# Performance work log

Measured on AMD Instinct MI355X. Metric: run time of the kernel, lower is better.

The kernel has to match this reference:

```python
import jax, jax.numpy as jnp
import numpy as np

B, NT, NZ, NX, NREC = 4, 256, 192, 192, 128
DT, DH = 0.001, 10.0


def setup_inputs() -> dict:
    key = jax.random.key(0)
    k1, k2, k3, k4 = jax.random.split(key, 4)
    # source wavelets, one trace per shot
    x = jax.random.normal(k1, (B, NT, 1), dtype=jnp.float32) * 1e2
    # realistic elastic media
    vp = 2500.0 + 1000.0 * jax.random.uniform(k2, (NZ, NX), dtype=jnp.float32)
    vs = vp / 1.78
    rho = 2000.0 + 300.0 * jax.random.uniform(k3, (NZ, NX), dtype=jnp.float32)
    # per-shot source location (z=5 near surface, random x)
    src_x = jax.random.randint(k4, (B,), 10, NX - 10)
    src_loc = jnp.stack([jnp.full((B,), 5), src_x], axis=1).astype(jnp.int32)
    # receiver line at depth z=5
    rec_x = jnp.linspace(10, NX - 10, NREC).astype(jnp.int32)
    rec_loc = jnp.stack([jnp.full((NREC,), 5, dtype=jnp.int32), rec_x], axis=1)
    return {"x": x, "vp": vp, "vs": vs, "rho": rho,
            "src_loc": src_loc, "rec_loc": rec_loc}


# staggered-grid first differences (forward / backward), zero-padded at edges
def _dxf(f):
    return jnp.pad(jnp.diff(f, axis=-1), ((0, 0), (0, 0), (0, 1))) / DH

def _dxb(f):
    return jnp.pad(jnp.diff(f, axis=-1), ((0, 0), (0, 0), (1, 0))) / DH

def _dzf(f):
    return jnp.pad(jnp.diff(f, axis=-2), ((0, 0), (0, 1), (0, 0))) / DH

def _dzb(f):
    return jnp.pad(jnp.diff(f, axis=-2), ((0, 0), (1, 0), (0, 0))) / DH


def _propagate(x, vp, vs, rho, src_loc, rec_loc):
    lam = rho * (vp ** 2 - 2.0 * vs ** 2)
    mu = rho * vs ** 2
    lam2mu = lam + 2.0 * mu
    buoy = DT / rho  # buoyancy * dt
    bidx = jnp.arange(B)
    sz, sx = src_loc[:, 0], src_loc[:, 1]
    rz, rx = rec_loc[:, 0], rec_loc[:, 1]

    def step(carry, wav_t):
        vx, vz, txx, tzz, txz = carry
        # velocity update from stress divergence
        vx = vx + buoy * (_dxf(txx) + _dzb(txz))
        vz = vz + buoy * (_dxb(txz) + _dzf(tzz))
        # stress update from velocity gradients
        dvxdx = _dxb(vx)
        dvzdz = _dzb(vz)
        txx = txx + DT * (lam2mu * dvxdx + lam * dvzdz)
        tzz = tzz + DT * (lam * dvxdx + lam2mu * dvzdz)
        txz = txz + DT * mu * (_dzf(vx) + _dxf(vz))
        # explosive source injection into txx, tzz (source_type = ['txx','tzz'])
        txx = txx.at[bidx, sz, sx].add(wav_t)
        tzz = tzz.at[bidx, sz, sx].add(wav_t)
        # probe extraction: (B, NREC)
        return (vx, vz, txx, tzz, txz), (vx[:, rz, rx], vz[:, rz, rx])

    z = jnp.zeros((B, NZ, NX), dtype=vp.dtype)
    _, (rvx, rvz) = jax.lax.scan(step, (z, z, z, z, z), x[:, :, 0].T)
    # torch: stack(dim=1) -> (B,NT,NREC); permute(1,2,0) -> (NT,NREC,B); cat dim=2
    y_vx = jnp.transpose(rvx, (0, 2, 1))  # (NT, NREC, B)
    y_vz = jnp.transpose(rvz, (0, 2, 1))
    return jnp.concatenate([y_vx, y_vz], axis=2)  # (NT, NREC, 2B)


def reference(x, vp, vs, rho, src_loc, rec_loc):
    return _propagate(x, vp, vs, rho, src_loc, rec_loc)
```

## Files before the change

kernel.cpp:

```cpp
#include <hip/hip_runtime.h>

#pragma clang fp contract(off)

#define B_    4
#define NT_   256
#define NZ_   192
#define NX_   192
#define NREC_ 128
#define DT_   0.001f
#define DH_   10.0f

#define N_CELL  (NZ_ * NX_)
#define N_FIELD (B_ * N_CELL)

#define K_     4
#define ROWS   4
#define NTHR   1024
#define VH     (2 * K_ - 1)
#define SH     (2 * K_)
#define VROWS  (ROWS + 2 * VH)
#define SROWS  (ROWS + 2 * SH)
#define TILES  (NZ_ / ROWS)
#define NBLK   (B_ * TILES)
#define LDS_BYTES ((2 * VROWS + 3 * SROWS) * NX_ * 4)

__device__ __forceinline__ int imax_(int a, int b) { return a > b ? a : b; }
__device__ __forceinline__ int imin_(int a, int b) { return a < b ? a : b; }

__global__ void mat_kernel(const float* __restrict__ vp, const float* __restrict__ vs,
                           const float* __restrict__ rho,
                           float* __restrict__ lam, float* __restrict__ dtmu,
                           float* __restrict__ lam2mu, float* __restrict__ buoy) {
    int i = blockIdx.x * blockDim.x + threadIdx.x;
    if (i >= N_CELL) return;
    float vpi = vp[i], vsi = vs[i], rhoi = rho[i];
    float vs2 = vsi * vsi;
    float mui = rhoi * vs2;
    float lami = rhoi * (vpi * vpi - 2.0f * vs2);
    lam[i] = lami;
    dtmu[i] = DT_ * mui;
    lam2mu[i] = lami + 2.0f * mui;
    buoy[i] = DT_ / rhoi;
}

template<int S>
__device__ __forceinline__ void substep(
    int tid, int z0, int base, int zv0, int zs0, int sz, int sx, int b, int t0,
    float* __restrict__ vxl, float* __restrict__ vzl,
    float* __restrict__ txxl, float* __restrict__ tzzl, float* __restrict__ txzl,
    const float* __restrict__ lam, const float* __restrict__ dtmu,
    const float* __restrict__ l2m, const float* __restrict__ buoy,
    const float* __restrict__ wav,
    bool rec_ok, int rec_idx, float* __restrict__ out,
    float* __restrict__ vxw, float* __restrict__ vzw,
    float* __restrict__ txxw, float* __restrict__ tzzw, float* __restrict__ txzw) {
    const int t = t0 + S;

    {
        constexpr int hv = 2 * (K_ - 1 - S) + 1;
        constexpr int IV = ((ROWS + 2 * hv) * NX_ + NTHR - 1) / NTHR;
        const int zlo = imax_(0, z0 - hv);
        const int zhi = imin_(NZ_ - 1, z0 + ROWS - 1 + hv);
        const int n   = (zhi - zlo + 1) * NX_;
#pragma unroll
        for (int it = 0; it < IV; ++it) {
            int idx = tid + it * NTHR;
            if (idx < n) {
                int dz = idx / NX_;
                int x  = idx - dz * NX_;
                int z  = zlo + dz;
                int zs = (z - zs0) * NX_ + x;
                int zr = (z - zv0) * NX_ + x;
                float txx_c = txxl[zs];
                float txz_c = txzl[zs];
                float dxf_txx = (x < NX_ - 1) ? (txxl[zs + 1] - txx_c) / DH_ : 0.0f;
                float dzb_txz = (z >= 1)      ? (txz_c - txzl[zs - NX_]) / DH_ : 0.0f;
                float dxb_txz = (x >= 1)      ? (txz_c - txzl[zs - 1]) / DH_ : 0.0f;
                float dzf_tzz = (z < NZ_ - 1) ? (tzzl[zs + NX_] - tzzl[zs]) / DH_ : 0.0f;
                float bu = buoy[z * NX_ + x];
                float nvx = vxl[zr] + bu * (dxf_txx + dzb_txz);
                float nvz = vzl[zr] + bu * (dxb_txz + dzf_tzz);
                vxl[zr] = nvx;
                vzl[zr] = nvz;
                if (S == K_ - 1) {
                    if (z >= z0 && z < z0 + ROWS) {
                        int g = base + z * NX_ + x;
                        vxw[g] = nvx;
                        vzw[g] = nvz;
                    }
                }
            }
        }
    }
    __syncthreads();

    if (rec_ok) {
        size_t o = ((size_t)t * NREC_ + tid) * (2 * B_);
        out[o + b]      = vxl[rec_idx];
        out[o + B_ + b] = vzl[rec_idx];
    }

    {
        constexpr int hs = 2 * (K_ - 1 - S);
        constexpr int IS = ((ROWS + 2 * hs) * NX_ + NTHR - 1) / NTHR;
        const int zlo = imax_(0, z0 - hs);
        const int zhi = imin_(NZ_ - 1, z0 + ROWS - 1 + hs);
        const int n   = (zhi - zlo + 1) * NX_;
#pragma unroll
        for (int it = 0; it < IS; ++it) {
            int idx = tid + it * NTHR;
            if (idx < n) {
                int dz = idx / NX_;
                int x  = idx - dz * NX_;
                int z  = zlo + dz;
                int zs = (z - zs0) * NX_ + x;
                int zr = (z - zv0) * NX_ + x;
                float vx_c = vxl[zr];
                float vz_c = vzl[zr];
                float dvxdx  = (x >= 1)      ? (vx_c - vxl[zr - 1]) / DH_ : 0.0f;
                float dvzdz  = (z >= 1)      ? (vz_c - vzl[zr - NX_]) / DH_ : 0.0f;
                float dzf_vx = (z < NZ_ - 1) ? (vxl[zr + NX_] - vx_c) / DH_ : 0.0f;
                float dxf_vz = (x < NX_ - 1) ? (vzl[zr + 1] - vz_c) / DH_ : 0.0f;
                int c = z * NX_ + x;
                float l  = lam[c];
                float lm = l2m[c];
                float ntxx = txxl[zs] + DT_ * (lm * dvxdx + l * dvzdz);
                float ntzz = tzzl[zs] + DT_ * (l * dvxdx + lm * dvzdz);
                float ntxz = txzl[zs] + dtmu[c] * (dzf_vx + dxf_vz);
                if (z == sz && x == sx) {
                    float w = wav[b * NT_ + t];
                    ntxx = ntxx + w;
                    ntzz = ntzz + w;
                }
                txxl[zs] = ntxx;
                tzzl[zs] = ntzz;
                txzl[zs] = ntxz;
                if (S == K_ - 1) {
                    int g = base + c;
                    txxw[g] = ntxx;
                    tzzw[g] = ntzz;
                    txzw[g] = ntxz;
                }
            }
        }
    }
    __syncthreads();
}

__global__ void __launch_bounds__(NTHR, 4)
step_kernel(const float* __restrict__ vxr, const float* __restrict__ vzr,
            const float* __restrict__ txxr, const float* __restrict__ tzzr,
            const float* __restrict__ txzr,
            float* __restrict__ vxw, float* __restrict__ vzw,
            float* __restrict__ txxw, float* __restrict__ tzzw, float* __restrict__ txzw,
            const float* __restrict__ lam, const float* __restrict__ dtmu,
            const float* __restrict__ l2m, const float* __restrict__ buoy,
            const float* __restrict__ wav, int t0,
            const int* __restrict__ src_loc, const int* __restrict__ rec_loc,
            float* __restrict__ out) {
    extern __shared__ float smem[];
    float* __restrict__ vxl  = smem;
    float* __restrict__ vzl  = vxl  + VROWS * NX_;
    float* __restrict__ txxl = vzl  + VROWS * NX_;
    float* __restrict__ tzzl = txxl + SROWS * NX_;
    float* __restrict__ txzl = tzzl + SROWS * NX_;

    const int tid  = threadIdx.x;
    const int b    = blockIdx.x / TILES;
    const int tile = blockIdx.x % TILES;
    const int z0   = tile * ROWS;
    const int base = b * N_CELL;
    const int zv0  = z0 - VH;
    const int zs0  = z0 - SH;

    const int sz = src_loc[2 * b];
    const int sx = src_loc[2 * b + 1];

    bool rec_ok = false;
    int rec_idx = 0;
    if (tid < NREC_) {
        int rz = rec_loc[2 * tid];
        int rx = rec_loc[2 * tid + 1];
        if (rz >= z0 && rz < z0 + ROWS) {
            rec_ok = true;
            rec_idx = (rz - zv0) * NX_ + rx;
        }
    }

#pragma unroll
    for (int idx = tid; idx < SROWS * NX_; idx += NTHR) {
        int zr = idx / NX_;
        int x  = idx - zr * NX_;
        int z  = zs0 + zr;
        if (z < 0 || z >= NZ_) continue;
        int g = base + z * NX_ + x;
        txxl[idx] = txxr[g];
        tzzl[idx] = tzzr[g];
        txzl[idx] = txzr[g];
    }
#pragma unroll
    for (int idx = tid; idx < VROWS * NX_; idx += NTHR) {
        int zr = idx / NX_;
        int x  = idx - zr * NX_;
        int z  = zv0 + zr;
        if (z < 0 || z >= NZ_) continue;
        int g = base + z * NX_ + x;
        vxl[idx] = vxr[g];
        vzl[idx] = vzr[g];
    }
    __syncthreads();

    substep<0>(tid, z0, base, zv0, zs0, sz, sx, b, t0, vxl, vzl, txxl, tzzl, txzl,
               lam, dtmu, l2m, buoy, wav, rec_ok, rec_idx, out, vxw, vzw, txxw, tzzw, txzw);
    substep<1>(tid, z0, base, zv0, zs0, sz, sx, b, t0, vxl, vzl, txxl, tzzl, txzl,
               lam, dtmu, l2m, buoy, wav, rec_ok, rec_idx, out, vxw, vzw, txxw, tzzw, txzw);
    substep<2>(tid, z0, base, zv0, zs0, sz, sx, b, t0, vxl, vzl, txxl, tzzl, txzl,
               lam, dtmu, l2m, buoy, wav, rec_ok, rec_idx, out, vxw, vzw, txxw, tzzw, txzw);
    substep<3>(tid, z0, base, zv0, zs0, sz, sx, b, t0, vxl, vzl, txxl, tzzl, txzl,
               lam, dtmu, l2m, buoy, wav, rec_ok, rec_idx, out, vxw, vzw, txxw, tzzw, txzw);
}

extern "C" void kernel_launch(void* const* d_in, const int* in_sizes, int n_in,
                              void* d_out, int out_size, void* d_ws, size_t ws_size,
                              hipStream_t stream) {
    const float* xw      = (const float*)d_in[0];
    const float* vp      = (const float*)d_in[1];
    const float* vs      = (const float*)d_in[2];
    const float* rho     = (const float*)d_in[3];
    const int*   src_loc = (const int*)d_in[4];
    const int*   rec_loc = (const int*)d_in[5];
    float*       out     = (float*)d_out;

    float* ws = (float*)d_ws;
    float* vx[2]  = { ws + 0 * N_FIELD, ws + 1 * N_FIELD };
    float* vz[2]  = { ws + 2 * N_FIELD, ws + 3 * N_FIELD };
    float* txx[2] = { ws + 4 * N_FIELD, ws + 5 * N_FIELD };
    float* tzz[2] = { ws + 6 * N_FIELD, ws + 7 * N_FIELD };
    float* txz[2] = { ws + 8 * N_FIELD, ws + 9 * N_FIELD };
    float* lam    = ws + 10 * N_FIELD;
    float* dtmu   = lam + N_CELL;
    float* l2m    = dtmu + N_CELL;
    float* buoy   = l2m + N_CELL;

    hipMemsetAsync(d_ws, 0, (size_t)10 * N_FIELD * sizeof(float), stream);

    mat_kernel<<<(N_CELL + 255) / 256, 256, 0, stream>>>(vp, vs, rho, lam, dtmu, l2m, buoy);

    for (int L = 0; L < NT_ / K_; ++L) {
        int p = L & 1;
        step_kernel<<<NBLK, NTHR, LDS_BYTES, stream>>>(
            vx[p], vz[p], txx[p], tzz[p], txz[p],
            vx[1 - p], vz[1 - p], txx[1 - p], tzz[1 - p], txz[1 - p],
            lam, dtmu, l2m, buoy,
            xw, L * K_, src_loc, rec_loc, out);
    }
}
```

Before: 1.193 ms.

## Vectorize stencil substeps with float4 per thread and shrink tile rows

Each thread now updates four consecutive x cells using float4 LDS and global loads/stores, replacing the strided scalar loops. Left and right neighbours come from the adjacent vector. ROWS drops from 4 to 3 so that the halo-extended tile (SROWS=19 rows × 48 vec4) fits in one pass of 1024 threads. The goal is fewer LDS instructions and less index arithmetic, at the cost of more blocks and more redundant halo work per useful row.

```diff
diff --git a/kernel.cpp b/kernel.cpp
--- a/kernel.cpp
+++ b/kernel.cpp
@@ -14,7 +14,7 @@
 #define N_FIELD (B_ * N_CELL)
 
 #define K_     4
-#define ROWS   4
+#define ROWS   3
 #define NTHR   1024
 #define VH     (2 * K_ - 1)
 #define SH     (2 * K_)
@@ -22,7 +22,10 @@
 #define SROWS  (ROWS + 2 * SH)
 #define TILES  (NZ_ / ROWS)
 #define NBLK   (B_ * TILES)
+#define NX4    (NX_ / 4)
 #define LDS_BYTES ((2 * VROWS + 3 * SROWS) * NX_ * 4)
+
+using f4 = __attribute__((ext_vector_type(4))) float;
 
 __device__ __forceinline__ int imax_(int a, int b) { return a > b ? a : b; }
 __device__ __forceinline__ int imin_(int a, int b) { return a < b ? a : b; }
@@ -58,36 +61,52 @@
 
     {
         constexpr int hv = 2 * (K_ - 1 - S) + 1;
-        constexpr int IV = ((ROWS + 2 * hv) * NX_ + NTHR - 1) / NTHR;
         const int zlo = imax_(0, z0 - hv);
         const int zhi = imin_(NZ_ - 1, z0 + ROWS - 1 + hv);
-        const int n   = (zhi - zlo + 1) * NX_;
+        const int n4  = (zhi - zlo + 1) * NX4;
+        if (tid < n4) {
+            int dz = tid / NX4;
+            int x4 = tid - dz * NX4;
+            int z  = zlo + dz;
+            int x0 = x4 * 4;
+            int zsrow = (z - zs0) * NX_;
+            int zvrow = (z - zv0) * NX_;
+            const f4* txxR = reinterpret_cast<const f4*>(txxl + zsrow);
+            const f4* txzR = reinterpret_cast<const f4*>(txzl + zsrow);
+            const f4* txzM = reinterpret_cast<const f4*>(txzl + zsrow - NX_);
+            const f4* tzzR = reinterpret_cast<const f4*>(tzzl + zsrow);
+            const f4* tzzP = reinterpret_cast<const f4*>(tzzl + zsrow + NX_);
+            f4 txo  = txxR[x4];
+            f4 txn  = txxR[x4 < NX4 - 1 ? x4 + 1 : x4];
+            f4 tzo  = txzR[x4];
+            f4 tzp  = txzR[x4 > 0 ? x4 - 1 : x4];
+            f4 tzm  = txzM[x4];
+            f4 tzzo = tzzR[x4];
+            f4 tzzp = tzzP[x4];
+            f4 vxo  = reinterpret_cast<const f4*>(vxl + zvrow)[x4];
+            f4 vzo  = reinterpret_cast<const f4*>(vzl + zvrow)[x4];
+            f4 bu   = *reinterpret_cast<const f4*>(buoy + z * NX_ + x0);
+            f4 nvx, nvz;
 #pragma unroll
-        for (int it = 0; it < IV; ++it) {
-            int idx = tid + it * NTHR;
-            if (idx < n) {
-                int dz = idx / NX_;
-                int x  = idx - dz * NX_;
-                int z  = zlo + dz;
-                int zs = (z - zs0) * NX_ + x;
-                int zr = (z - zv0) * NX_ + x;
-                float txx_c = txxl[zs];
-                float txz_c = txzl[zs];
-                float dxf_txx = (x < NX_ - 1) ? (txxl[zs + 1] - txx_c) / DH_ : 0.0f;
-                float dzb_txz = (z >= 1)      ? (txz_c - txzl[zs - NX_]) / DH_ : 0.0f;
-                float dxb_txz = (x >= 1)      ? (txz_c - txzl[zs - 1]) / DH_ : 0.0f;
-                float dzf_tzz = (z < NZ_ - 1) ? (tzzl[zs + NX_] - tzzl[zs]) / DH_ : 0.0f;
-                float bu = buoy[z * NX_ + x];
-                float nvx = vxl[zr] + bu * (dxf_txx + dzb_txz);
-                float nvz = vzl[zr] + bu * (dxb_txz + dzf_tzz);
-                vxl[zr] = nvx;
-                vzl[zr] = nvz;
-                if (S == K_ - 1) {
-                    if (z >= z0 && z < z0 + ROWS) {
-                        int g = base + z * NX_ + x;
-                        vxw[g] = nvx;
-                        vzw[g] = nvz;
-                    }
+            for (int e = 0; e < 4; ++e) {
+                int xg = x0 + e;
+                float txx_c = txo[e];
+                float txxp1 = (e == 3) ? txn[0] : txo[e + 1];
+                float txz_c = tzo[e];
+                float txzm1 = (e == 0) ? tzp[3] : tzo[e - 1];
+                float dxf_txx = (xg < NX_ - 1) ? (txxp1 - txx_c) / DH_ : 0.0f;
+                float dzb_txz = (z >= 1)       ? (txz_c - tzm[e]) / DH_ : 0.0f;
+                float dxb_txz = (xg >= 1)      ? (txz_c - txzm1) / DH_ : 0.0f;
+                float dzf_tzz = (z < NZ_ - 1)  ? (tzzp[e] - tzzo[e]) / DH_ : 0.0f;
+                nvx[e] = vxo[e] + bu[e] * (dxf_txx + dzb_txz);
+                nvz[e] = vzo[e] + bu[e] * (dxb_txz + dzf_tzz);
+            }
+            reinterpret_cast<f4*>(vxl + zvrow)[x4] = nvx;
+            reinterpret_cast<f4*>(vzl + zvrow)[x4] = nvz;
+            if (S == K_ - 1) {
+                if (z >= z0 && z < z0 + ROWS) {
+                    *reinterpret_cast<f4*>(vxw + base + z * NX_ + x0) = nvx;
+                    *reinterpret_cast<f4*>(vzw + base + z * NX_ + x0) = nvz;
                 }
             }
         }
@@ -102,45 +121,59 @@
 
     {
         constexpr int hs = 2 * (K_ - 1 - S);
-        constexpr int IS = ((ROWS + 2 * hs) * NX_ + NTHR - 1) / NTHR;
         const int zlo = imax_(0, z0 - hs);
         const int zhi = imin_(NZ_ - 1, z0 + ROWS - 1 + hs);
-        const int n   = (zhi - zlo + 1) * NX_;
+        const int n4  = (zhi - zlo + 1) * NX4;
+        if (tid < n4) {
+            int dz = tid / NX4;
+            int x4 = tid - dz * NX4;
+            int z  = zlo + dz;
+            int x0 = x4 * 4;
+            int zsrow = (z - zs0) * NX_;
+            int zvrow = (z - zv0) * NX_;
+            const f4* vxR = reinterpret_cast<const f4*>(vxl + zvrow);
+            const f4* vxP = reinterpret_cast<const f4*>(vxl + zvrow + NX_);
+            const f4* vzR = reinterpret_cast<const f4*>(vzl + zvrow);
+            const f4* vzM = reinterpret_cast<const f4*>(vzl + zvrow - NX_);
+            f4 vxo  = vxR[x4];
+            f4 vxp  = vxR[x4 > 0 ? x4 - 1 : x4];
+            f4 vxzp = vxP[x4];
+            f4 vzo  = vzR[x4];
+            f4 vzn  = vzR[x4 < NX4 - 1 ? x4 + 1 : x4];
+            f4 vzm  = vzM[x4];
+            f4 txxo = reinterpret_cast<const f4*>(txxl + zsrow)[x4];
+            f4 tzzo = reinterpret_cast<const f4*>(tzzl + zsrow)[x4];
+            f4 txzo = reinterpret_cast<const f4*>(txzl + zsrow)[x4];
+            int c0 = z * NX_ + x0;
+            f4 l   = *reinterpret_cast<const f4*>(lam  + c0);
+            f4 lm  = *reinterpret_cast<const f4*>(l2m  + c0);
+            f4 dtm = *reinterpret_cast<const f4*>(dtmu + c0);
+            float w = wav[b * NT_ + t];
+            f4 ntxx, ntzz, ntxz;
 #pragma unroll
-        for (int it = 0; it < IS; ++it) {
-            int idx = tid + it * NTHR;
-            if (idx < n) {
-                int dz = idx / NX_;
-                int x  = idx - dz * NX_;
-                int z  = zlo + dz;
-                int zs = (z - zs0) * NX_ + x;
-                int zr = (z - zv0) * NX_ + x;
-                float vx_c = vxl[zr];
-                float vz_c = vzl[zr];
-                float dvxdx  = (x >= 1)      ? (vx_c - vxl[zr - 1]) / DH_ : 0.0f;
-                float dvzdz  = (z >= 1)      ? (vz_c - vzl[zr - NX_]) / DH_ : 0.0f;
-                float dzf_vx = (z < NZ_ - 1) ? (vxl[zr + NX_] - vx_c) / DH_ : 0.0f;
-                float dxf_vz = (x < NX_ - 1) ? (vzl[zr + 1] - vz_c) / DH_ : 0.0f;
-                int c = z * NX_ + x;
-                float l  = lam[c];
-                float lm = l2m[c];
-                float ntxx = txxl[zs] + DT_ * (lm * dvxdx + l * dvzdz);
-                float ntzz = tzzl[zs] + DT_ * (l * dvxdx + lm * dvzdz);
-                float ntxz = txzl[zs] + dtmu[c] * (dzf_vx + dxf_vz);
-                if (z == sz && x == sx) {
-                    float w = wav[b * NT_ + t];
-                    ntxx = ntxx + w;
-                    ntzz = ntzz + w;
-                }
-                txxl[zs] = ntxx;
-                tzzl[zs] = ntzz;
-                txzl[zs] = ntxz;
-                if (S == K_ - 1) {
-                    int g = base + c;
-                    txxw[g] = ntxx;
-                    tzzw[g] = ntzz;
-                    txzw[g] = ntxz;
-                }
+            for (int e = 0; e < 4; ++e) {
+                int xg = x0 + e;
+                float vx_c = vxo[e];
+                float vz_c = vzo[e];
+                float vxm1 = (e == 0) ? vxp[3] : vxo[e - 1];
+                float vzp1 = (e == 3) ? vzn[0] : vzo[e + 1];
+                float dvxdx  = (xg >= 1)      ? (vx_c - vxm1) / DH_ : 0.0f;
+                float dvzdz  = (z >= 1)       ? (vz_c - vzm[e]) / DH_ : 0.0f;
+                float dzf_vx = (z < NZ_ - 1)  ? (vxzp[e] - vx_c) / DH_ : 0.0f;
+                float dxf_vz = (xg < NX_ - 1) ? (vzp1 - vz_c) / DH_ : 0.0f;
+                float a  = txxo[e] + DT_ * (lm[e] * dvxdx + l[e] * dvzdz);
+                float bb = tzzo[e] + DT_ * (l[e] * dvxdx + lm[e] * dvzdz);
+                float cc = txzo[e] + dtm[e] * (dzf_vx + dxf_vz);
+                if (z == sz && xg == sx) { a = a + w; bb = bb + w; }
+                ntxx[e] = a; ntzz[e] = bb; ntxz[e] = cc;
+            }
+            reinterpret_cast<f4*>(txxl + zsrow)[x4] = ntxx;
+            reinterpret_cast<f4*>(tzzl + zsrow)[x4] = ntzz;
+            reinterpret_cast<f4*>(txzl + zsrow)[x4] = ntxz;
+            if (S == K_ - 1) {
+                *reinterpret_cast<f4*>(txxw + base + c0) = ntxx;
+                *reinterpret_cast<f4*>(tzzw + base + c0) = ntzz;
+                *reinterpret_cast<f4*>(txzw + base + c0) = ntxz;
             }
         }
     }
@@ -187,26 +220,26 @@
         }
     }
 
-#pragma unroll
-    for (int idx = tid; idx < SROWS * NX_; idx += NTHR) {
-        int zr = idx / NX_;
-        int x  = idx - zr * NX_;
-        int z  = zs0 + zr;
-        if (z < 0 || z >= NZ_) continue;
-        int g = base + z * NX_ + x;
-        txxl[idx] = txxr[g];
-        tzzl[idx] = tzzr[g];
-        txzl[idx] = txzr[g];
-    }
-#pragma unroll
-    for (int idx = tid; idx < VROWS * NX_; idx += NTHR) {
-        int zr = idx / NX_;
-        int x  = idx - zr * NX_;
-        int z  = zv0 + zr;
-        if (z < 0 || z >= NZ_) continue;
-        int g = base + z * NX_ + x;
-        vxl[idx] = vxr[g];
-        vzl[idx] = vzr[g];
+    if (tid < SROWS * NX4) {
+        int dz = tid / NX4;
+        int x4 = tid - dz * NX4;
+        int z  = zs0 + dz;
+        if (z >= 0 && z < NZ_) {
+            int g = base + z * NX_ + x4 * 4;
+            reinterpret_cast<f4*>(txxl)[tid] = *reinterpret_cast<const f4*>(txxr + g);
+            reinterpret_cast<f4*>(tzzl)[tid] = *reinterpret_cast<const f4*>(tzzr + g);
+            reinterpret_cast<f4*>(txzl)[tid] = *reinterpret_cast<const f4*>(txzr + g);
+        }
+    }
+    if (tid < VROWS * NX4) {
+        int dz = tid / NX4;
+        int x4 = tid - dz * NX4;
+        int z  = zv0 + dz;
+        if (z >= 0 && z < NZ_) {
+            int g = base + z * NX_ + x4 * 4;
+            reinterpret_cast<f4*>(vxl)[tid] = *reinterpret_cast<const f4*>(vxr + g);
+            reinterpret_cast<f4*>(vzl)[tid] = *reinterpret_cast<const f4*>(vzr + g);
+        }
     }
     __syncthreads();
 
```

Result: no change. 1.198 ms (+0.4%).

## Keep per-thread 4-wide field strip in registers with vectorized LDS stencil

Applied to the files above, without the earlier changes.

Each thread now owns one row and a 4-column strip of the tile. Its field values and material coefficients stay in float4 registers across the four fused substeps. Neighbours are read from LDS with vector loads, and all global and LDS traffic is 128-bit. ROWS drops to 3 so that SROWS*48 threads fit within 1024. This adds halo recompute per tile and launches more blocks, but removes scalar index math and repeated global reads of the material arrays.

```diff
diff --git a/kernel.cpp b/kernel.cpp
--- a/kernel.cpp
+++ b/kernel.cpp
@@ -14,7 +14,7 @@
 #define N_FIELD (B_ * N_CELL)
 
 #define K_     4
-#define ROWS   4
+#define ROWS   3
 #define NTHR   1024
 #define VH     (2 * K_ - 1)
 #define SH     (2 * K_)
@@ -22,10 +22,10 @@
 #define SROWS  (ROWS + 2 * SH)
 #define TILES  (NZ_ / ROWS)
 #define NBLK   (B_ * TILES)
+#define NX4    (NX_ / 4)
 #define LDS_BYTES ((2 * VROWS + 3 * SROWS) * NX_ * 4)
 
-__device__ __forceinline__ int imax_(int a, int b) { return a > b ? a : b; }
-__device__ __forceinline__ int imin_(int a, int b) { return a < b ? a : b; }
+using f4 = __attribute__((ext_vector_type(4))) float;
 
 __global__ void mat_kernel(const float* __restrict__ vp, const float* __restrict__ vs,
                            const float* __restrict__ rho,
@@ -40,54 +40,53 @@
     lam[i] = lami;
     dtmu[i] = DT_ * mui;
     lam2mu[i] = lami + 2.0f * mui;
+    buoy[i] = DT_ * (1.0f / rhoi);
     buoy[i] = DT_ / rhoi;
 }
 
 template<int S>
 __device__ __forceinline__ void substep(
-    int tid, int z0, int base, int zv0, int zs0, int sz, int sx, int b, int t0,
+    bool zin, int z, int srow, int x4, int x0, int z0, int sz, int sx, int b, int t0,
+    f4& r_vx, f4& r_vz, f4& r_txx, f4& r_tzz, f4& r_txz,
+    const f4& m_bu, const f4& m_l, const f4& m_lm, const f4& m_dtm,
     float* __restrict__ vxl, float* __restrict__ vzl,
     float* __restrict__ txxl, float* __restrict__ tzzl, float* __restrict__ txzl,
-    const float* __restrict__ lam, const float* __restrict__ dtmu,
-    const float* __restrict__ l2m, const float* __restrict__ buoy,
     const float* __restrict__ wav,
-    bool rec_ok, int rec_idx, float* __restrict__ out,
-    float* __restrict__ vxw, float* __restrict__ vzw,
+    bool rec_ok, int rec_idx, int tid, float* __restrict__ out,
+    int base, float* __restrict__ vxw, float* __restrict__ vzw,
     float* __restrict__ txxw, float* __restrict__ tzzw, float* __restrict__ txzw) {
     const int t = t0 + S;
+    const int sOff = srow * NX_ + x0;
+    const int vOff = (srow - 1) * NX_ + x0;
 
     {
         constexpr int hv = 2 * (K_ - 1 - S) + 1;
-        constexpr int IV = ((ROWS + 2 * hv) * NX_ + NTHR - 1) / NTHR;
-        const int zlo = imax_(0, z0 - hv);
-        const int zhi = imin_(NZ_ - 1, z0 + ROWS - 1 + hv);
-        const int n   = (zhi - zlo + 1) * NX_;
+        bool act = zin && (z >= z0 - hv) && (z <= z0 + ROWS - 1 + hv);
+        if (act) {
+            f4 txn  = *reinterpret_cast<const f4*>(txxl + sOff + (x4 < NX4 - 1 ? 4 : 0));
+            f4 tzp  = *reinterpret_cast<const f4*>(txzl + sOff - (x4 > 0 ? 4 : 0));
+            f4 tzm  = *reinterpret_cast<const f4*>(txzl + sOff - NX_);
+            f4 tzzp = *reinterpret_cast<const f4*>(tzzl + sOff + NX_);
 #pragma unroll
-        for (int it = 0; it < IV; ++it) {
-            int idx = tid + it * NTHR;
-            if (idx < n) {
-                int dz = idx / NX_;
-                int x  = idx - dz * NX_;
-                int z  = zlo + dz;
-                int zs = (z - zs0) * NX_ + x;
-                int zr = (z - zv0) * NX_ + x;
-                float txx_c = txxl[zs];
-                float txz_c = txzl[zs];
-                float dxf_txx = (x < NX_ - 1) ? (txxl[zs + 1] - txx_c) / DH_ : 0.0f;
-                float dzb_txz = (z >= 1)      ? (txz_c - txzl[zs - NX_]) / DH_ : 0.0f;
-                float dxb_txz = (x >= 1)      ? (txz_c - txzl[zs - 1]) / DH_ : 0.0f;
-                float dzf_tzz = (z < NZ_ - 1) ? (tzzl[zs + NX_] - tzzl[zs]) / DH_ : 0.0f;
-                float bu = buoy[z * NX_ + x];
-                float nvx = vxl[zr] + bu * (dxf_txx + dzb_txz);
-                float nvz = vzl[zr] + bu * (dxb_txz + dzf_tzz);
-                vxl[zr] = nvx;
-                vzl[zr] = nvz;
-                if (S == K_ - 1) {
-                    if (z >= z0 && z < z0 + ROWS) {
-                        int g = base + z * NX_ + x;
-                        vxw[g] = nvx;
-                        vzw[g] = nvz;
-                    }
+            for (int e = 0; e < 4; ++e) {
+                int xg = x0 + e;
+                float txx_c = r_txx[e];
+                float txxp1 = (e == 3) ? txn[0] : r_txx[e + 1];
+                float txz_c = r_txz[e];
+                float txzm1 = (e == 0) ? tzp[3] : r_txz[e - 1];
+                float dxf_txx = (xg < NX_ - 1) ? (txxp1 - txx_c) / DH_ : 0.0f;
+                float dzb_txz = (z >= 1)       ? (txz_c - tzm[e]) / DH_ : 0.0f;
+                float dxb_txz = (xg >= 1)      ? (txz_c - txzm1) / DH_ : 0.0f;
+                float dzf_tzz = (z < NZ_ - 1)  ? (tzzp[e] - r_tzz[e]) / DH_ : 0.0f;
+                r_vx[e] = r_vx[e] + m_bu[e] * (dxf_txx + dzb_txz);
+                r_vz[e] = r_vz[e] + m_bu[e] * (dxb_txz + dzf_tzz);
+            }
+            *reinterpret_cast<f4*>(vxl + vOff) = r_vx;
+            *reinterpret_cast<f4*>(vzl + vOff) = r_vz;
+            if (S == K_ - 1) {
+                if (z >= z0 && z < z0 + ROWS) {
+                    *reinterpret_cast<f4*>(vxw + base + z * NX_ + x0) = r_vx;
+                    *reinterpret_cast<f4*>(vzw + base + z * NX_ + x0) = r_vz;
                 }
             }
         }
@@ -102,45 +101,38 @@
 
     {
         constexpr int hs = 2 * (K_ - 1 - S);
-        constexpr int IS = ((ROWS + 2 * hs) * NX_ + NTHR - 1) / NTHR;
-        const int zlo = imax_(0, z0 - hs);
-        const int zhi = imin_(NZ_ - 1, z0 + ROWS - 1 + hs);
-        const int n   = (zhi - zlo + 1) * NX_;
+        bool act = zin && (z >= z0 - hs) && (z <= z0 + ROWS - 1 + hs);
+        if (act) {
+            f4 vxp  = *reinterpret_cast<const f4*>(vxl + vOff - (x4 > 0 ? 4 : 0));
+            f4 vxzp = *reinterpret_cast<const f4*>(vxl + vOff + NX_);
+            f4 vzn  = *reinterpret_cast<const f4*>(vzl + vOff + (x4 < NX4 - 1 ? 4 : 0));
+            f4 vzm  = *reinterpret_cast<const f4*>(vzl + vOff - NX_);
+            float w = wav[b * NT_ + t];
 #pragma unroll
-        for (int it = 0; it < IS; ++it) {
-            int idx = tid + it * NTHR;
-            if (idx < n) {
-                int dz = idx / NX_;
-                int x  = idx - dz * NX_;
-                int z  = zlo + dz;
-                int zs = (z - zs0) * NX_ + x;
-                int zr = (z - zv0) * NX_ + x;
-                float vx_c = vxl[zr];
-                float vz_c = vzl[zr];
-                float dvxdx  = (x >= 1)      ? (vx_c - vxl[zr - 1]) / DH_ : 0.0f;
-                float dvzdz  = (z >= 1)      ? (vz_c - vzl[zr - NX_]) / DH_ : 0.0f;
-                float dzf_vx = (z < NZ_ - 1) ? (vxl[zr + NX_] - vx_c) / DH_ : 0.0f;
-                float dxf_vz = (x < NX_ - 1) ? (vzl[zr + 1] - vz_c) / DH_ : 0.0f;
-                int c = z * NX_ + x;
-                float l  = lam[c];
-                float lm = l2m[c];
-                float ntxx = txxl[zs] + DT_ * (lm * dvxdx + l * dvzdz);
-                float ntzz = tzzl[zs] + DT_ * (l * dvxdx + lm * dvzdz);
-                float ntxz = txzl[zs] + dtmu[c] * (dzf_vx + dxf_vz);
-                if (z == sz && x == sx) {
-                    float w = wav[b * NT_ + t];
-                    ntxx = ntxx + w;
-                    ntzz = ntzz + w;
-                }
-                txxl[zs] = ntxx;
-                tzzl[zs] = ntzz;
-                txzl[zs] = ntxz;
-                if (S == K_ - 1) {
-                    int g = base + c;
-                    txxw[g] = ntxx;
-                    tzzw[g] = ntzz;
-                    txzw[g] = ntxz;
-                }
+            for (int e = 0; e < 4; ++e) {
+                int xg = x0 + e;
+                float vx_c = r_vx[e];
+                float vz_c = r_vz[e];
+                float vxm1 = (e == 0) ? vxp[3] : r_vx[e - 1];
+                float vzp1 = (e == 3) ? vzn[0] : r_vz[e + 1];
+                float dvxdx  = (xg >= 1)      ? (vx_c - vxm1) / DH_ : 0.0f;
+                float dvzdz  = (z >= 1)       ? (vz_c - vzm[e]) / DH_ : 0.0f;
+                float dzf_vx = (z < NZ_ - 1)  ? (vxzp[e] - vx_c) / DH_ : 0.0f;
+                float dxf_vz = (xg < NX_ - 1) ? (vzp1 - vz_c) / DH_ : 0.0f;
+                float a  = r_txx[e] + DT_ * (m_lm[e] * dvxdx + m_l[e] * dvzdz);
+                float bb = r_tzz[e] + DT_ * (m_l[e] * dvxdx + m_lm[e] * dvzdz);
+                float cc = r_txz[e] + m_dtm[e] * (dzf_vx + dxf_vz);
+                if (z == sz && xg == sx) { a = a + w; bb = bb + w; }
+                r_txx[e] = a; r_tzz[e] = bb; r_txz[e] = cc;
+            }
+            *reinterpret_cast<f4*>(txxl + sOff) = r_txx;
+            *reinterpret_cast<f4*>(tzzl + sOff) = r_tzz;
+            *reinterpret_cast<f4*>(txzl + sOff) = r_txz;
+            if (S == K_ - 1) {
+                int g = base + z * NX_ + x0;
+                *reinterpret_cast<f4*>(txxw + g) = r_txx;
+                *reinterpret_cast<f4*>(tzzw + g) = r_tzz;
+                *reinterpret_cast<f4*>(txzw + g) = r_txz;
             }
         }
     }
@@ -176,6 +168,13 @@
     const int sz = src_loc[2 * b];
     const int sx = src_loc[2 * b + 1];
 
+    const int srow = tid / NX4;
+    const int x4   = tid - srow * NX4;
+    const int x0   = x4 * 4;
+    const int z    = zs0 + srow;
+    const bool zin = (srow < SROWS) && (z >= 0) && (z < NZ_);
+    const bool vin = zin && srow >= 1 && srow <= VROWS;
+
     bool rec_ok = false;
     int rec_idx = 0;
     if (tid < NREC_) {
@@ -187,37 +186,44 @@
         }
     }
 
-#pragma unroll
-    for (int idx = tid; idx < SROWS * NX_; idx += NTHR) {
-        int zr = idx / NX_;
-        int x  = idx - zr * NX_;
-        int z  = zs0 + zr;
-        if (z < 0 || z >= NZ_) continue;
-        int g = base + z * NX_ + x;
-        txxl[idx] = txxr[g];
-        tzzl[idx] = tzzr[g];
-        txzl[idx] = txzr[g];
-    }
-#pragma unroll
-    for (int idx = tid; idx < VROWS * NX_; idx += NTHR) {
-        int zr = idx / NX_;
-        int x  = idx - zr * NX_;
-        int z  = zv0 + zr;
-        if (z < 0 || z >= NZ_) continue;
-        int g = base + z * NX_ + x;
-        vxl[idx] = vxr[g];
-        vzl[idx] = vzr[g];
+    f4 r_vx = {0,0,0,0}, r_vz = {0,0,0,0}, r_txx = {0,0,0,0}, r_tzz = {0,0,0,0}, r_txz = {0,0,0,0};
+    f4 m_bu = {0,0,0,0}, m_l = {0,0,0,0}, m_lm = {0,0,0,0}, m_dtm = {0,0,0,0};
+    if (zin) {
+        int g = base + z * NX_ + x0;
+        int c = z * NX_ + x0;
+        r_txx = *reinterpret_cast<const f4*>(txxr + g);
+        r_tzz = *reinterpret_cast<const f4*>(tzzr + g);
+        r_txz = *reinterpret_cast<const f4*>(txzr + g);
+        m_bu  = *reinterpret_cast<const f4*>(buoy + c);
+        m_l   = *reinterpret_cast<const f4*>(lam  + c);
+        m_lm  = *reinterpret_cast<const f4*>(l2m  + c);
+        m_dtm = *reinterpret_cast<const f4*>(dtmu + c);
+        int sOff = srow * NX_ + x0;
+        *reinterpret_cast<f4*>(txxl + sOff) = r_txx;
+        *reinterpret_cast<f4*>(tzzl + sOff) = r_tzz;
+        *reinterpret_cast<f4*>(txzl + sOff) = r_txz;
+        if (vin) {
+            r_vx = *reinterpret_cast<const f4*>(vxr + g);
+            r_vz = *reinterpret_cast<const f4*>(vzr + g);
+            int vOff = (srow - 1) * NX_ + x0;
+            *reinterpret_cast<f4*>(vxl + vOff) = r_vx;
+            *reinterpret_cast<f4*>(vzl + vOff) = r_vz;
+        }
     }
     __syncthreads();
 
-    substep<0>(tid, z0, base, zv0, zs0, sz, sx, b, t0, vxl, vzl, txxl, tzzl, txzl,
-               lam, dtmu, l2m, buoy, wav, rec_ok, rec_idx, out, vxw, vzw, txxw, tzzw, txzw);
-    substep<1>(tid, z0, base, zv0, zs0, sz, sx, b, t0, vxl, vzl, txxl, tzzl, txzl,
-               lam, dtmu, l2m, buoy, wav, rec_ok, rec_idx, out, vxw, vzw, txxw, tzzw, txzw);
-    substep<2>(tid, z0, base, zv0, zs0, sz, sx, b, t0, vxl, vzl, txxl, tzzl, txzl,
-               lam, dtmu, l2m, buoy, wav, rec_ok, rec_idx, out, vxw, vzw, txxw, tzzw, txzw);
-    substep<3>(tid, z0, base, zv0, zs0, sz, sx, b, t0, vxl, vzl, txxl, tzzl, txzl,
-               lam, dtmu, l2m, buoy, wav, rec_ok, rec_idx, out, vxw, vzw, txxw, tzzw, txzw);
+    substep<0>(zin, z, srow, x4, x0, z0, sz, sx, b, t0, r_vx, r_vz, r_txx, r_tzz, r_txz,
+               m_bu, m_l, m_lm, m_dtm, vxl, vzl, txxl, tzzl, txzl,
+               wav, rec_ok, rec_idx, tid, out, base, vxw, vzw, txxw, tzzw, txzw);
+    substep<1>(zin, z, srow, x4, x0, z0, sz, sx, b, t0, r_vx, r_vz, r_txx, r_tzz, r_txz,
+               m_bu, m_l, m_lm, m_dtm, vxl, vzl, txxl, tzzl, txzl,
+               wav, rec_ok, rec_idx, tid, out, base, vxw, vzw, txxw, tzzw, txzw);
+    substep<2>(zin, z, srow, x4, x0, z0, sz, sx, b, t0, r_vx, r_vz, r_txx, r_tzz, r_txz,
+               m_bu, m_l, m_lm, m_dtm, vxl, vzl, txxl, tzzl, txzl,
+               wav, rec_ok, rec_idx, tid, out, base, vxw, vzw, txxw, tzzw, txzw);
+    substep<3>(zin, z, srow, x4, x0, z0, sz, sx, b, t0, r_vx, r_vz, r_txx, r_tzz, r_txz,
+               m_bu, m_l, m_lm, m_dtm, vxl, vzl, txxl, tzzl, txzl,
+               wav, rec_ok, rec_idx, tid, out, base, vxw, vzw, txxw, tzzw, txzw);
 }
 
 extern "C" void kernel_launch(void* const* d_in, const int* in_sizes, int n_in,
```

Result: faster. 1.154 ms (-3.3%).
